# Kernel optimization log

Measured on AMD Instinct MI355X. Metric: run time of the kernel, lower is better.

The kernel has to match this reference:

```python
import jax, jax.numpy as jnp
import numpy as np

NUM_HEADS = 16
ROPE_THETA = 10000.0


def _rope_cos_sin(T, head_dim, dtype):
    # inv_freq over even indices; cos/sin shape [T, head_dim//2]
    inv_freq = 1.0 / (ROPE_THETA ** (jnp.arange(0, head_dim, 2, dtype=jnp.float32) / head_dim))
    t = jnp.arange(T, dtype=jnp.float32)
    freqs = jnp.outer(t, inv_freq)  # [T, hd/2]
    return jnp.cos(freqs).astype(dtype), jnp.sin(freqs).astype(dtype)


def _apply_rope(x, cos, sin):
    # x: [B,H,T,hd]; de-interleave even/odd, rotate, concat halves
    x1 = x[..., ::2]
    x2 = x[..., 1::2]
    return jnp.concatenate([x1 * cos - x2 * sin, x1 * sin + x2 * cos], axis=-1)


def setup_inputs() -> dict:
    key = jax.random.key(0)
    k1, k2, k3 = jax.random.split(key, 3)
    B, T, C = 2, 2048, 2048
    x = jax.random.normal(k1, (B, T, C), dtype=jnp.float32)
    w_qkv = jax.random.normal(k2, (3 * C, C), dtype=jnp.float32) * (C ** -0.5)
    w_proj = jax.random.normal(k3, (C, C), dtype=jnp.float32) * (C ** -0.5)
    causal_mask = jnp.tril(jnp.ones((T, T), dtype=bool))[None, None, :, :]  # [1,1,T,T]
    return {"x": x, "w_qkv": w_qkv, "w_proj": w_proj, "causal_mask": causal_mask}


def reference(x, w_qkv, w_proj, causal_mask):
    B, T, C = x.shape
    H = NUM_HEADS
    hd = C // H
    scale = hd ** -0.5

    qkv = jnp.einsum('btc,oc->bto', x, w_qkv)  # [B,T,3C]
    qkv = qkv.reshape(B, T, 3, H, hd).transpose(2, 0, 3, 1, 4)  # [3,B,H,T,hd]
    q, k, v = qkv[0], qkv[1], qkv[2]

    cos, sin = _rope_cos_sin(T, hd, x.dtype)
    q = _apply_rope(q, cos, sin)
    k = _apply_rope(k, cos, sin)

    scores = jnp.einsum('bhqd,bhkd->bhqk', q, k) * scale  # [B,H,T,T]
    scores = jnp.where(causal_mask, scores, -jnp.inf)
    attn = jax.nn.softmax(scores, axis=-1)
    out = jnp.einsum('bhqk,bhkd->bhqd', attn, v)  # [B,H,T,hd]
    out = out.transpose(0, 2, 1, 3).reshape(B, T, C)
    return jnp.einsum('btc,oc->bto', out, w_proj)
```

## Files before the change

kernel.cpp:

```cpp
#include <hip/hip_runtime.h>
#include <stdint.h>

typedef float f32x4 __attribute__((ext_vector_type(4)));
typedef __bf16 bf16x8 __attribute__((ext_vector_type(8)));
typedef unsigned short u16x8 __attribute__((ext_vector_type(8)));

__device__ __forceinline__ unsigned short f2bf(float f) {
  union { float f; unsigned u; } x; x.f = f;
  unsigned r = x.u + 0x7fffu + ((x.u >> 16) & 1u);
  return (unsigned short)(r >> 16);
}
__device__ __forceinline__ float bf2f(unsigned short u) {
  union { unsigned u; float f; } x; x.u = ((unsigned)u) << 16;
  return x.f;
}
__device__ __forceinline__ void async_copy16(void* lds, const void* g) {
  __builtin_amdgcn_global_load_lds(
      (const unsigned int __attribute__((address_space(1)))*)g,
      (unsigned int __attribute__((address_space(3)))*)lds, 16, 0, 0);
}
__device__ __forceinline__ f32x4 mfma16(bf16x8 a, bf16x8 b, f32x4 c) {
  return __builtin_amdgcn_mfma_f32_16x16x32_bf16(a, b, c, 0, 0, 0);
}

__global__ __launch_bounds__(256) void cvt_f32_bf16(
    const float* __restrict__ in, unsigned short* __restrict__ out, int n8) {
  int stride = gridDim.x * blockDim.x;
  for (int i = blockIdx.x * blockDim.x + threadIdx.x; i < n8; i += stride) {
    const float4* p = (const float4*)in + (size_t)i * 2;
    float4 a = p[0], b = p[1];
    u16x8 o;
    o[0] = f2bf(a.x); o[1] = f2bf(a.y); o[2] = f2bf(a.z); o[3] = f2bf(a.w);
    o[4] = f2bf(b.x); o[5] = f2bf(b.y); o[6] = f2bf(b.z); o[7] = f2bf(b.w);
    *((u16x8*)out + i) = o;
  }
}

__global__ __launch_bounds__(256) void rope_table(float2* __restrict__ cs) {
  int idx = blockIdx.x * 256 + threadIdx.x;
  if (idx >= 2048 * 64) return;
  int t = idx >> 6, j = idx & 63;
  float inv = expf(-0.14391156516026f * (float)j);
  float ang = (float)t * inv;
  cs[idx] = make_float2(cosf(ang), sinf(ang));
}

template <bool OUT_F32>
__global__ __launch_bounds__(512, 2) void gemm_dp(
    const unsigned short* __restrict__ A, const unsigned short* __restrict__ Bt,
    void* __restrict__ Cout, int M, int N, int K) {
  __shared__ unsigned short sA[3][128 * 64];
  __shared__ unsigned short sB[3][256 * 64];
  const int tid = threadIdx.x;
  const int w = tid >> 6, l = tid & 63;
  const int wm = w >> 2, wn = w & 3;
  const int g = l >> 4, lr = l & 15;
  const int m0 = blockIdx.y * 128, n0 = blockIdx.x * 256;

  f32x4 acc[4][4];
#pragma unroll
  for (int i = 0; i < 4; ++i)
#pragma unroll
    for (int j = 0; j < 4; ++j) acc[i][j] = f32x4{0.f, 0.f, 0.f, 0.f};

  auto stageA = [&](int buf, int kt) {
    const int k0 = kt * 64;
#pragma unroll
    for (int i = 0; i < 2; ++i) {
      int u = i * 512 + tid;
      int row = u >> 3, sl = u & 7;
      int sg = sl ^ (row & 7);
      async_copy16(&sA[buf][u * 8], A + (size_t)(m0 + row) * K + k0 + sg * 8);
    }
  };
  auto stageB = [&](int buf, int kt, int half) {
    const int k0 = kt * 64;
#pragma unroll
    for (int i = 0; i < 2; ++i) {
      int u = (half * 2 + i) * 512 + tid;
      int row = u >> 3, sl = u & 7;
      int sg = sl ^ (row & 7);
      async_copy16(&sB[buf][u * 8], Bt + (size_t)(n0 + row) * K + k0 + sg * 8);
    }
  };

  const int NK = K / 64;
  stageA(0, 0); stageB(0, 0, 0); stageB(0, 0, 1);
  stageA(1, 1); stageB(1, 1, 0); stageB(1, 1, 1);

  for (int kt = 0; kt < NK; ++kt) {
    const int cur = kt % 3, nxt = (kt + 2) % 3;
    if (kt + 1 < NK) asm volatile("s_waitcnt vmcnt(6)" ::: "memory");
    else             asm volatile("s_waitcnt vmcnt(0)" ::: "memory");
    __builtin_amdgcn_s_barrier();

    bf16x8 bq[4][2], af0[2][2];
#pragma unroll
    for (int ni = 0; ni < 4; ++ni) {
      int row = wn * 64 + ni * 16 + lr;
#pragma unroll
      for (int kk = 0; kk < 2; ++kk)
        bq[ni][kk] = *(const bf16x8*)&sB[cur][row * 64 +
                       (((kk * 4 + g) ^ (row & 7)) << 3)];
    }
#pragma unroll
    for (int mi = 0; mi < 2; ++mi) {
      int row = wm * 64 + mi * 16 + lr;
#pragma unroll
      for (int kk = 0; kk < 2; ++kk)
        af0[mi][kk] = *(const bf16x8*)&sA[cur][row * 64 +
                        (((kk * 4 + g) ^ (row & 7)) << 3)];
    }
    if (kt + 2 < NK) { stageA(nxt, kt + 2); stageB(nxt, kt + 2, 0); }
    __builtin_amdgcn_s_barrier();
    __builtin_amdgcn_s_setprio(1);
#pragma unroll
    for (int kk = 0; kk < 2; ++kk)
#pragma unroll
      for (int mi = 0; mi < 2; ++mi)
#pragma unroll
        for (int ni = 0; ni < 4; ++ni)
          acc[mi][ni] = mfma16(af0[mi][kk], bq[ni][kk], acc[mi][ni]);
    __builtin_amdgcn_s_setprio(0);

    bf16x8 af1[2][2];
#pragma unroll
    for (int mi = 0; mi < 2; ++mi) {
      int row = wm * 64 + (2 + mi) * 16 + lr;
#pragma unroll
      for (int kk = 0; kk < 2; ++kk)
        af1[mi][kk] = *(const bf16x8*)&sA[cur][row * 64 +
                        (((kk * 4 + g) ^ (row & 7)) << 3)];
    }
    if (kt + 2 < NK) stageB(nxt, kt + 2, 1);
    __builtin_amdgcn_s_barrier();
    __builtin_amdgcn_s_setprio(1);
#pragma unroll
    for (int kk = 0; kk < 2; ++kk)
#pragma unroll
      for (int mi = 0; mi < 2; ++mi)
#pragma unroll
        for (int ni = 0; ni < 4; ++ni)
          acc[2 + mi][ni] = mfma16(af1[mi][kk], bq[ni][kk], acc[2 + mi][ni]);
    __builtin_amdgcn_s_setprio(0);
  }

#pragma unroll
  for (int mi = 0; mi < 4; ++mi)
#pragma unroll
    for (int ni = 0; ni < 4; ++ni) {
      int col = n0 + wn * 64 + ni * 16 + lr;
#pragma unroll
      for (int jr = 0; jr < 4; ++jr) {
        int row = m0 + wm * 64 + mi * 16 + g * 4 + jr;
        float v = acc[mi][ni][jr];
        if (OUT_F32)
          ((float*)Cout)[(size_t)row * N + col] = v;
        else
          ((unsigned short*)Cout)[(size_t)row * N + col] = f2bf(v);
      }
    }
}

__global__ __launch_bounds__(256) void prep_rope(
    const unsigned short* __restrict__ qkv, const float2* __restrict__ cs,
    unsigned short* __restrict__ Q, unsigned short* __restrict__ K,
    unsigned short* __restrict__ Vt) {
  const int tt = blockIdx.x, h = blockIdx.y, b = blockIdx.z;
  const int t0 = tt * 64;
  const int tid = threadIdx.x;
  __shared__ unsigned short vt[64][130];

#pragma unroll 4
  for (int i = 0; i < 32; ++i) {
    int lin = i * 256 + tid;
    int r = lin >> 7, j = lin & 127;
    int t = t0 + r;
    int jj = j & 63;
    size_t rowbase = ((size_t)(b * 2048 + t)) * 6144 + h * 128;
    float2 c_s = cs[t * 64 + jj];
    float q1 = bf2f(qkv[rowbase + 2 * jj]);
    float q2 = bf2f(qkv[rowbase + 2 * jj + 1]);
    float k1 = bf2f(qkv[rowbase + 2048 + 2 * jj]);
    float k2 = bf2f(qkv[rowbase + 2048 + 2 * jj + 1]);
    float qo = (j < 64) ? (q1 * c_s.x - q2 * c_s.y) : (q1 * c_s.y + q2 * c_s.x);
    float ko = (j < 64) ? (k1 * c_s.x - k2 * c_s.y) : (k1 * c_s.y + k2 * c_s.x);
    size_t obase = ((size_t)((b * 16 + h) * 2048 + t)) * 128 + j;
    Q[obase] = f2bf(qo);
    K[obase] = f2bf(ko);
    vt[r][j] = qkv[rowbase + 4096 + j];
  }
  __syncthreads();
  size_t vbase = ((size_t)((b * 16 + h) * 128)) * 2048 + t0;
#pragma unroll 4
  for (int i = 0; i < 32; ++i) {
    int lin = i * 256 + tid;
    int d = lin >> 6, c = lin & 63;
    Vt[vbase + (size_t)d * 2048 + c] = vt[c][d];
  }
}

__global__ __launch_bounds__(512, 2) void attn_fwd(
    const unsigned short* __restrict__ Q, const unsigned short* __restrict__ K,
    const unsigned short* __restrict__ Vt, unsigned short* __restrict__ AO) {
  const int bid = blockIdx.x;
  const int bh = (bid & 7) * 4 + ((bid >> 3) & 3);
  const int qp = bid >> 5;
  const int b = bh >> 4, h = bh & 15;
  __shared__ unsigned short sK[2][64 * 128];
  __shared__ unsigned short sV[2][128 * 64];
  __shared__ unsigned short sP[8][16 * 64];
  const int tid = threadIdx.x, w = tid >> 6, l = tid & 63;
  const int g = l >> 4, lr = l & 15;
  const size_t qkbase = (size_t)bh * 2048 * 128;
  const size_t vbase = (size_t)bh * 128 * 2048;
  const float scale = 0.08838834764831845f;

  auto stage = [&](int buf, int kt) {
#pragma unroll
    for (int j = 0; j < 2; ++j) {
      int r = w * 2 + j;
      int kv = r * 4 + (l >> 4);
      int sc = (l & 15) ^ (kv & 15);
      async_copy16(&sK[buf][r * 512],
                   K + qkbase + (size_t)(kt * 64 + kv) * 128 + sc * 8);
      int d = r * 8 + (l >> 3);
      int sv = (l & 7) ^ (d & 7);
      async_copy16(&sV[buf][r * 512],
                   Vt + vbase + (size_t)d * 2048 + kt * 64 + sv * 8);
    }
  };

  auto process = [&](int qt) {
    const int q0w = qt * 128 + w * 16;
    bf16x8 qf[4];
#pragma unroll
    for (int kc = 0; kc < 4; ++kc)
      qf[kc] = *(const bf16x8*)(Q + qkbase + (size_t)(q0w + lr) * 128 +
                                kc * 32 + g * 8);
    f32x4 of[8];
    float mrow[4], lsum[4];
#pragma unroll
    for (int nd = 0; nd < 8; ++nd) of[nd] = f32x4{0.f, 0.f, 0.f, 0.f};
#pragma unroll
    for (int jr = 0; jr < 4; ++jr) { mrow[jr] = -1e30f; lsum[jr] = 0.f; }

    const int NT = 2 * qt + 2;
    __syncthreads();
    stage(0, 0);
    int cur = 0;
    for (int kt = 0; kt < NT; ++kt) {
      asm volatile("s_waitcnt vmcnt(0)" ::: "memory");
      __syncthreads();
      if (kt + 1 < NT) stage(cur ^ 1, kt + 1);

      if (kt * 64 <= q0w + 15) {
        f32x4 sacc[4];
#pragma unroll
        for (int ni = 0; ni < 4; ++ni) sacc[ni] = f32x4{0.f, 0.f, 0.f, 0.f};
#pragma unroll
        for (int kc = 0; kc < 4; ++kc)
#pragma unroll
          for (int ni = 0; ni < 4; ++ni) {
            int kv = ni * 16 + lr;
            bf16x8 kf = *(const bf16x8*)&sK[cur][kv * 128 +
                          (((kc * 4 + g) ^ (kv & 15)) << 3)];
            sacc[ni] = mfma16(qf[kc], kf, sacc[ni]);
          }

        const bool needmask = (kt * 64 + 63 > q0w);
        float pm[4] = {-1e30f, -1e30f, -1e30f, -1e30f};
#pragma unroll
        for (int ni = 0; ni < 4; ++ni)
#pragma unroll
          for (int jr = 0; jr < 4; ++jr) {
            float sv = sacc[ni][jr] * scale;
            if (needmask) {
              int kvg = kt * 64 + ni * 16 + lr;
              int qg = q0w + g * 4 + jr;
              if (kvg > qg) sv = -1e30f;
            }
            sacc[ni][jr] = sv;
            pm[jr] = fmaxf(pm[jr], sv);
          }
#pragma unroll
        for (int jr = 0; jr < 4; ++jr) {
          float v = pm[jr];
          v = fmaxf(v, __shfl_xor(v, 1));
          v = fmaxf(v, __shfl_xor(v, 2));
          v = fmaxf(v, __shfl_xor(v, 4));
          v = fmaxf(v, __shfl_xor(v, 8));
          float mnew = fmaxf(mrow[jr], v);
          float fac = __expf(mrow[jr] - mnew);
          mrow[jr] = mnew;
          float rsum = 0.f;
#pragma unroll
          for (int ni = 0; ni < 4; ++ni) {
            float p = __expf(sacc[ni][jr] - mnew);
            sacc[ni][jr] = p;
            rsum += p;
          }
          rsum += __shfl_xor(rsum, 1);
          rsum += __shfl_xor(rsum, 2);
          rsum += __shfl_xor(rsum, 4);
          rsum += __shfl_xor(rsum, 8);
          lsum[jr] = lsum[jr] * fac + rsum;
#pragma unroll
          for (int nd = 0; nd < 8; ++nd) of[nd][jr] *= fac;
        }

#pragma unroll
        for (int ni = 0; ni < 4; ++ni)
#pragma unroll
          for (int jr = 0; jr < 4; ++jr) {
            int q = g * 4 + jr;
            int kv = ni * 16 + lr;
            sP[w][q * 64 + (((kv >> 3) ^ (q & 7)) << 3) + (kv & 7)] =
                f2bf(sacc[ni][jr]);
          }

#pragma unroll
        for (int kc = 0; kc < 2; ++kc) {
          bf16x8 pa = *(const bf16x8*)&sP[w][lr * 64 +
                        (((kc * 4 + g) ^ (lr & 7)) << 3)];
#pragma unroll
          for (int nd = 0; nd < 8; ++nd) {
            int d = nd * 16 + lr;
            bf16x8 vb = *(const bf16x8*)&sV[cur][d * 64 +
                          (((kc * 4 + g) ^ (d & 7)) << 3)];
            of[nd] = mfma16(pa, vb, of[nd]);
          }
        }
      }
      cur ^= 1;
    }

#pragma unroll
    for (int nd = 0; nd < 8; ++nd)
#pragma unroll
      for (int jr = 0; jr < 4; ++jr) {
        int qrow = q0w + g * 4 + jr;
        int d = nd * 16 + lr;
        AO[(size_t)(b * 2048 + qrow) * 2048 + h * 128 + d] =
            f2bf(of[nd][jr] / lsum[jr]);
      }
  };

  process(qp);
  process(15 - qp);
}

extern "C" void kernel_launch(void* const* d_in, const int* in_sizes, int n_in,
                              void* d_out, int out_size, void* d_ws, size_t ws_size,
                              hipStream_t stream) {
  (void)in_sizes; (void)n_in; (void)out_size; (void)ws_size;
  const float* x = (const float*)d_in[0];
  const float* wqkv = (const float*)d_in[1];
  const float* wproj = (const float*)d_in[2];

  char* ws = (char*)d_ws;
  unsigned short* WPROJB = (unsigned short*)(ws + 0);
  unsigned short* XB     = (unsigned short*)(ws + 8388608);
  unsigned short* WQKVB  = (unsigned short*)(ws + 25165824);
  unsigned short* QKV    = (unsigned short*)(ws + 50331648);
  unsigned short* Kr     = (unsigned short*)(ws + 100663296);
  unsigned short* Vt     = (unsigned short*)(ws + 117440512);
  float2*         CS     = (float2*)(ws + 134217728);
  unsigned short* AO = XB;
  unsigned short* Qr = WQKVB;

  rope_table<<<512, 256, 0, stream>>>(CS);
  cvt_f32_bf16<<<2048, 256, 0, stream>>>(x, XB, 8388608 / 8);
  cvt_f32_bf16<<<2048, 256, 0, stream>>>(wqkv, WQKVB, 12582912 / 8);
  cvt_f32_bf16<<<1024, 256, 0, stream>>>(wproj, WPROJB, 4194304 / 8);
  gemm_dp<false><<<dim3(24, 32), 512, 0, stream>>>(XB, WQKVB, QKV, 4096, 6144, 2048);
  prep_rope<<<dim3(32, 16, 2), 256, 0, stream>>>(QKV, CS, Qr, Kr, Vt);
  attn_fwd<<<256, 512, 0, stream>>>(Qr, Kr, Vt, AO);
  gemm_dp<true><<<dim3(8, 32), 512, 0, stream>>>(AO, WPROJB, d_out, 4096, 2048, 2048);
}
```

Before: 423.6 us.

## Add 256x256-tile GEMM with interleaved half-tile staging for QKV projection

Adds a new GEMM kernel using 256x256 output tiles (8x4 MFMA accumulators per wave) and double-buffered LDS. It splits each k-step into four MFMA phases, and the async global-to-LDS copy for the next tiles is issued in halves between them, with setprio around the MFMA bursts. Only the QKV projection uses it, with half as many blocks as before. The larger tile raises arithmetic intensity and cuts global traffic. The cost is more registers per thread, 64 KB of LDS per block, fewer blocks (384) on the machine and more barriers per k-step.

```diff
diff --git a/kernel.cpp b/kernel.cpp
--- a/kernel.cpp
+++ b/kernel.cpp
@@ -43,6 +43,150 @@
   float inv = expf(-0.14391156516026f * (float)j);
   float ang = (float)t * inv;
   cs[idx] = make_float2(cosf(ang), sinf(ang));
+}
+
+template <bool OUT_F32>
+__global__ __launch_bounds__(512, 2) void gemm8(
+    const unsigned short* __restrict__ A, const unsigned short* __restrict__ Bt,
+    void* __restrict__ Cout, int M, int N, int K) {
+  __shared__ unsigned short sA[2][256 * 64];
+  __shared__ unsigned short sB[2][256 * 64];
+  const int tid = threadIdx.x;
+  const int w = tid >> 6, l = tid & 63;
+  const int wm = w >> 2, wn = w & 3;
+  const int g = l >> 4, lr = l & 15;
+  const int m0 = blockIdx.y * 256, n0 = blockIdx.x * 256;
+
+  f32x4 acc[8][4];
+#pragma unroll
+  for (int i = 0; i < 8; ++i)
+#pragma unroll
+    for (int j = 0; j < 4; ++j) acc[i][j] = f32x4{0.f, 0.f, 0.f, 0.f};
+
+  auto stageH = [&](const unsigned short* src, int base0, unsigned short* dst,
+                    int kt, int half) {
+    const int k0 = kt * 64;
+#pragma unroll
+    for (int i = 0; i < 2; ++i) {
+      int u = i * 512 + tid;
+      int row = half * 128 + (u >> 3), sl = u & 7;
+      int sg = sl ^ (row & 7);
+      async_copy16(dst + (size_t)half * 8192 + (size_t)u * 8,
+                   src + (size_t)(base0 + row) * K + k0 + sg * 8);
+    }
+  };
+  auto rdA = [&](int c, int mi, int kk) {
+    int row = wm * 128 + mi * 16 + lr;
+    return *(const bf16x8*)&sA[c][row * 64 + (((kk * 4 + g) ^ (row & 7)) << 3)];
+  };
+  auto rdB = [&](int c, int ni, int kk) {
+    int row = wn * 64 + ni * 16 + lr;
+    return *(const bf16x8*)&sB[c][row * 64 + (((kk * 4 + g) ^ (row & 7)) << 3)];
+  };
+
+  const int NK = K / 64;
+  stageH(A, m0, sA[0], 0, 0);
+  stageH(A, m0, sA[0], 0, 1);
+  stageH(Bt, n0, sB[0], 0, 0);
+  stageH(Bt, n0, sB[0], 0, 1);
+  if (NK > 1) {
+    stageH(A, m0, sA[1], 1, 0);
+    asm volatile("s_waitcnt vmcnt(2)" ::: "memory");
+  } else {
+    asm volatile("s_waitcnt vmcnt(0)" ::: "memory");
+  }
+  __builtin_amdgcn_s_barrier();
+
+  for (int t = 0; t < NK; ++t) {
+    const int c = t & 1, nb = c ^ 1;
+    bf16x8 af[4][2], bfr[4][2];
+
+#pragma unroll
+    for (int mi = 0; mi < 4; ++mi)
+#pragma unroll
+      for (int kk = 0; kk < 2; ++kk) af[mi][kk] = rdA(c, mi, kk);
+#pragma unroll
+    for (int ni = 0; ni < 2; ++ni)
+#pragma unroll
+      for (int kk = 0; kk < 2; ++kk) bfr[ni][kk] = rdB(c, ni, kk);
+    if (t + 1 < NK) stageH(A, m0, sA[nb], t + 1, 1);
+    __builtin_amdgcn_s_barrier();
+    __builtin_amdgcn_s_setprio(1);
+#pragma unroll
+    for (int kk = 0; kk < 2; ++kk)
+#pragma unroll
+      for (int mi = 0; mi < 4; ++mi)
+#pragma unroll
+        for (int ni = 0; ni < 2; ++ni)
+          acc[mi][ni] = mfma16(af[mi][kk], bfr[ni][kk], acc[mi][ni]);
+    __builtin_amdgcn_s_setprio(0);
+    __builtin_amdgcn_s_barrier();
+
+#pragma unroll
+    for (int ni = 2; ni < 4; ++ni)
+#pragma unroll
+      for (int kk = 0; kk < 2; ++kk) bfr[ni][kk] = rdB(c, ni, kk);
+    if (t + 1 < NK) stageH(Bt, n0, sB[nb], t + 1, 0);
+    __builtin_amdgcn_s_barrier();
+    __builtin_amdgcn_s_setprio(1);
+#pragma unroll
+    for (int kk = 0; kk < 2; ++kk)
+#pragma unroll
+      for (int mi = 0; mi < 4; ++mi)
+#pragma unroll
+        for (int ni = 2; ni < 4; ++ni)
+          acc[mi][ni] = mfma16(af[mi][kk], bfr[ni][kk], acc[mi][ni]);
+    __builtin_amdgcn_s_setprio(0);
+    __builtin_amdgcn_s_barrier();
+
+#pragma unroll
+    for (int mi = 0; mi < 4; ++mi)
+#pragma unroll
+      for (int kk = 0; kk < 2; ++kk) af[mi][kk] = rdA(c, 4 + mi, kk);
+    if (t + 1 < NK) stageH(Bt, n0, sB[nb], t + 1, 1);
+    __builtin_amdgcn_s_barrier();
+    __builtin_amdgcn_s_setprio(1);
+#pragma unroll
+    for (int kk = 0; kk < 2; ++kk)
+#pragma unroll
+      for (int mi = 0; mi < 4; ++mi)
+#pragma unroll
+        for (int ni = 0; ni < 2; ++ni)
+          acc[4 + mi][ni] = mfma16(af[mi][kk], bfr[ni][kk], acc[4 + mi][ni]);
+    __builtin_amdgcn_s_setprio(0);
+    __builtin_amdgcn_s_barrier();
+
+    if (t + 2 < NK) stageH(A, m0, sA[c], t + 2, 0);
+    __builtin_amdgcn_s_barrier();
+    __builtin_amdgcn_s_setprio(1);
+#pragma unroll
+    for (int kk = 0; kk < 2; ++kk)
+#pragma unroll
+      for (int mi = 0; mi < 4; ++mi)
+#pragma unroll
+        for (int ni = 2; ni < 4; ++ni)
+          acc[4 + mi][ni] = mfma16(af[mi][kk], bfr[ni][kk], acc[4 + mi][ni]);
+    __builtin_amdgcn_s_setprio(0);
+    if (t + 2 < NK) asm volatile("s_waitcnt vmcnt(2)" ::: "memory");
+    else            asm volatile("s_waitcnt vmcnt(0)" ::: "memory");
+    __builtin_amdgcn_s_barrier();
+  }
+
+#pragma unroll
+  for (int mi = 0; mi < 8; ++mi)
+#pragma unroll
+    for (int ni = 0; ni < 4; ++ni) {
+      int col = n0 + wn * 64 + ni * 16 + lr;
+#pragma unroll
+      for (int jr = 0; jr < 4; ++jr) {
+        int row = m0 + wm * 128 + mi * 16 + g * 4 + jr;
+        float v = acc[mi][ni][jr];
+        if (OUT_F32)
+          ((float*)Cout)[(size_t)row * N + col] = v;
+        else
+          ((unsigned short*)Cout)[(size_t)row * N + col] = f2bf(v);
+      }
+    }
 }
 
 template <bool OUT_F32>
@@ -373,7 +517,7 @@
   cvt_f32_bf16<<<2048, 256, 0, stream>>>(x, XB, 8388608 / 8);
   cvt_f32_bf16<<<2048, 256, 0, stream>>>(wqkv, WQKVB, 12582912 / 8);
   cvt_f32_bf16<<<1024, 256, 0, stream>>>(wproj, WPROJB, 4194304 / 8);
-  gemm_dp<false><<<dim3(24, 32), 512, 0, stream>>>(XB, WQKVB, QKV, 4096, 6144, 2048);
+  gemm8<false><<<dim3(24, 16), 512, 0, stream>>>(XB, WQKVB, QKV, 4096, 6144, 2048);
   prep_rope<<<dim3(32, 16, 2), 256, 0, stream>>>(QKV, CS, Qr, Kr, Vt);
   attn_fwd<<<256, 512, 0, stream>>>(Qr, Kr, Vt, AO);
   gemm_dp<true><<<dim3(8, 32), 512, 0, stream>>>(AO, WPROJB, d_out, 4096, 2048, 2048);
```

New measurement: 430.2 us. About the same (+1.5%).
